# Optimization experiments

Measured on AMD Instinct MI355X. Metric: run time of the kernel, lower is better.

The kernel has to match this reference:

```python
import jax, jax.numpy as jnp
import numpy as np
from jax import lax

B, L = 128, 256
DW, DC = 100, 30
H = 400          # hidden_size (bidirectional total)
HD = H // 2      # per-direction hidden
NT = 18          # tag vocab size (BIOES)
VW, VC = 400000, 50000


def setup_inputs():
    key = jax.random.key(0)
    ks = iter(jax.random.split(key, 64))
    rn = lambda shape, s=0.1: jax.random.normal(next(ks), shape, jnp.float32) * s
    inp = {
        "words": jax.random.randint(next(ks), (B, L), 0, VW),
        "cap_words": jax.random.randint(next(ks), (B, L), 0, VC),
        "seq_len": jax.random.randint(next(ks), (B,), L // 2, L + 1),
        "target": jax.random.randint(next(ks), (B, L), 0, NT),
        "word_emb": rn((VW, DW)),
        "char_emb": rn((VC, DC)),
    }
    for l, din in ((0, DW + DC), (1, H)):
        for d in ("f", "b"):
            inp[f"W_ih_l{l}{d}"] = rn((4 * HD, din))
            inp[f"W_hh_l{l}{d}"] = rn((4 * HD, HD))
            inp[f"b_ih_l{l}{d}"] = rn((4 * HD,))
            inp[f"b_hh_l{l}{d}"] = rn((4 * HD,))
    inp["Wf"], inp["bf"] = rn((NT, HD)), jnp.zeros((NT,), jnp.float32)
    inp["Wb"], inp["bb"] = rn((NT, HD)), jnp.zeros((NT,), jnp.float32)
    inp["trans"] = rn((NT, NT))
    return inp


def _lstm_dir(x, W_ih, W_hh, b_ih, b_hh):
    # x: [B, L, D] -> hidden states [B, L, HD]; torch gate order i, f, g, o
    Bsz = x.shape[0]
    def step(carry, xt):
        h, c = carry
        g = xt @ W_ih.T + b_ih + h @ W_hh.T + b_hh
        i, f, gg, o = jnp.split(g, 4, axis=-1)
        c = jax.nn.sigmoid(f) * c + jax.nn.sigmoid(i) * jnp.tanh(gg)
        h = jax.nn.sigmoid(o) * jnp.tanh(c)
        return (h, c), h
    init = (jnp.zeros((Bsz, HD), x.dtype), jnp.zeros((Bsz, HD), x.dtype))
    _, hs = lax.scan(step, init, jnp.swapaxes(x, 0, 1))
    return jnp.swapaxes(hs, 0, 1)


def _rev(x, seq_len):
    # reverse each sequence within its true length (padding stays in place),
    # emulating pack_padded_sequence semantics for the backward direction
    t = jnp.arange(x.shape[1])[None, :]
    idx = jnp.where(t < seq_len[:, None], seq_len[:, None] - 1 - t, t)
    return jnp.take_along_axis(x, idx[:, :, None], axis=1)


def _crf_nll(logits, tags, mask, trans):
    # normalizer: forward algorithm, logsumexp scan over time with mask
    def step(alpha, inp):
        emit, m = inp  # emit: [B, NT], m: [B] bool
        new = jax.nn.logsumexp(alpha[:, :, None] + trans[None] + emit[:, None, :], axis=1)
        return jnp.where(m[:, None], new, alpha), None
    emits = jnp.swapaxes(logits, 0, 1)  # [L, B, NT]
    ms = jnp.swapaxes(mask, 0, 1)
    alpha, _ = lax.scan(step, emits[0], (emits[1:], ms[1:]))
    z = jax.nn.logsumexp(alpha, axis=1)
    # gold path score
    mf = mask.astype(logits.dtype)
    emit_sc = jnp.take_along_axis(logits, tags[:, :, None], axis=2)[:, :, 0]
    gold = jnp.sum(emit_sc * mf, axis=1) + jnp.sum(trans[tags[:, :-1], tags[:, 1:]] * mf[:, 1:], axis=1)
    return z - gold  # per-sample negative log-likelihood, shape [B]


def _model(words, cap_words, seq_len, target, word_emb, char_emb,
           W_ih_l0f, W_hh_l0f, b_ih_l0f, b_hh_l0f, W_ih_l0b, W_hh_l0b, b_ih_l0b, b_hh_l0b,
           W_ih_l1f, W_hh_l1f, b_ih_l1f, b_hh_l1f, W_ih_l1b, W_hh_l1b, b_ih_l1b, b_hh_l1b,
           Wf, bf, Wb, bb, trans):
    mask = jnp.arange(L)[None, :] < seq_len[:, None]  # [B, L] bool
    mf = mask.astype(jnp.float32)[:, :, None]
    x = jnp.concatenate([word_emb[words], char_emb[cap_words]], axis=-1)
    layers = (((W_ih_l0f, W_hh_l0f, b_ih_l0f, b_hh_l0f), (W_ih_l0b, W_hh_l0b, b_ih_l0b, b_hh_l0b)),
              ((W_ih_l1f, W_hh_l1f, b_ih_l1f, b_hh_l1f), (W_ih_l1b, W_hh_l1b, b_ih_l1b, b_hh_l1b)))
    h = x
    for fp, bp in layers:
        fwd = _lstm_dir(h, *fp)
        bwd = _rev(_lstm_dir(_rev(h, seq_len), *bp), seq_len)
        h = jnp.concatenate([fwd, bwd], axis=-1) * mf  # zero padded steps like packed LSTM
    forwards, backwards = h[..., :HD], h[..., HD:]
    logits = forwards @ Wf.T + bf + backwards @ Wb.T + bb
    return _crf_nll(logits, target, mask, trans)


def reference(words, cap_words, seq_len, target, word_emb, char_emb,
              W_ih_l0f, W_hh_l0f, b_ih_l0f, b_hh_l0f, W_ih_l0b, W_hh_l0b, b_ih_l0b, b_hh_l0b,
              W_ih_l1f, W_hh_l1f, b_ih_l1f, b_hh_l1f, W_ih_l1b, W_hh_l1b, b_ih_l1b, b_hh_l1b,
              Wf, bf, Wb, bb, trans):
    return _model(words, cap_words, seq_len, target, word_emb, char_emb,
                  W_ih_l0f, W_hh_l0f, b_ih_l0f, b_hh_l0f, W_ih_l0b, W_hh_l0b, b_ih_l0b, b_hh_l0b,
                  W_ih_l1f, W_hh_l1f, b_ih_l1f, b_hh_l1f, W_ih_l1b, W_hh_l1b, b_ih_l1b, b_hh_l1b,
                  Wf, bf, Wb, bb, trans)
```

## Files before the change

### kernel.cpp

```cpp
#include <hip/hip_runtime.h>
#include <math.h>

#define B_   128
#define L_   256
#define DW_  100
#define DC_  30
#define HD_  200
#define NT_  18
#define SG   4
#define KP0  160
#define KP1  416
#define WLP  424

typedef _Float16 half8 __attribute__((ext_vector_type(8)));
typedef _Float16 half4 __attribute__((ext_vector_type(4)));
typedef float    f32x4 __attribute__((ext_vector_type(4)));

__device__ __forceinline__ float frcp_(float x) { return __builtin_amdgcn_rcpf(x); }
__device__ __forceinline__ float sigm_(float x) { return frcp_(1.0f + __expf(-x)); }
__device__ __forceinline__ float tanh_(float x) { return 1.0f - 2.0f * frcp_(1.0f + __expf(2.0f * x)); }

__device__ __forceinline__ void barrier_lgkm() {
    asm volatile("s_waitcnt lgkmcnt(0)" ::: "memory");
    __builtin_amdgcn_s_barrier();
    asm volatile("" ::: "memory");
}

__global__ __launch_bounds__(128) void k_sortperm(const int* __restrict__ seq_len,
                                                  int* __restrict__ perm) {
    __shared__ int s[B_];
    int i = threadIdx.x;
    s[i] = seq_len[i];
    __syncthreads();
    int key = s[i], r = 0;
    for (int j = 0; j < B_; j++) {
        int v = s[j];
        r += (v < key) || (v == key && j < i);
    }
    perm[r] = i;
}

__global__ void k_embed(const int* __restrict__ words, const int* __restrict__ caps,
                        const float* __restrict__ wemb, const float* __restrict__ cemb,
                        _Float16* __restrict__ x) {
    int pos = blockIdx.x;
    int w = words[pos], c = caps[pos];
    _Float16* xp = x + (size_t)pos * KP0;
    for (int t = threadIdx.x; t < KP0; t += blockDim.x) {
        float v = 0.f;
        if (t < DW_) v = wemb[(size_t)w * DW_ + t];
        else if (t < DW_ + DC_) v = cemb[(size_t)c * DC_ + (t - DW_)];
        xp[t] = (_Float16)v;
    }
}

__global__ void k_perm_ih16(const float* __restrict__ src, _Float16* __restrict__ dst,
                            int K, int Kpad, int colOff) {
    int i = blockIdx.x * blockDim.x + threadIdx.x;
    if (i >= 800 * Kpad) return;
    int r = i / Kpad, k = i - r * Kpad;
    int jh = r % 200, g = r / 200;
    int col = colOff + (jh << 2) + g;
    dst[(size_t)col * Kpad + k] = (k < K) ? (_Float16)src[(size_t)r * K + k] : (_Float16)0.f;
}

__global__ void k_bias_perm(const float* bi_f, const float* bh_f,
                            const float* bi_b, const float* bh_b, float* bias) {
    int j = blockIdx.x * blockDim.x + threadIdx.x;
    if (j >= 1600) return;
    int dir = j / 800, r = j - dir * 800;
    int col = dir * 800 + ((r % 200) << 2) + (r / 200);
    bias[col] = dir ? (bi_b[r] + bh_b[r]) : (bi_f[r] + bh_f[r]);
}

__global__ void k_wlog(const float* __restrict__ Wf, const float* __restrict__ bfv,
                       const float* __restrict__ Wb, const float* __restrict__ bbv,
                       _Float16* __restrict__ wlB, float* __restrict__ blog) {
    int i = blockIdx.x * blockDim.x + threadIdx.x;
    if (i < 32 * WLP) {
        int n = i / WLP, k = i - n * WLP;
        float v = 0.f;
        if (n < NT_ && k < 400) v = (k < HD_) ? Wf[n * HD_ + k] : Wb[n * HD_ + (k - HD_)];
        wlB[i] = (_Float16)v;
    }
    if (i < NT_) blog[i] = bfv[i] + bbv[i];
}

__global__ __launch_bounds__(256) void k_gemm16(const _Float16* __restrict__ A,
                                                const _Float16* __restrict__ Bt,
                                                const float* __restrict__ bias,
                                                _Float16* __restrict__ C,
                                                int Kpad) {
    __shared__ __align__(16) _Float16 smem[128 * 72];
    _Float16* sA = smem;
    _Float16* sB = smem + 128 * 40;
    const int tid = threadIdx.x;
    const int w = tid >> 6, l = tid & 63, l15 = l & 15, lq = l >> 4;
    const int m0 = blockIdx.y * 128, n0 = blockIdx.x * 64;
    const int rw = (w >> 1) * 64, cw = (w & 1) * 32;
    f32x4 acc[4][2];
    #pragma unroll
    for (int i = 0; i < 4; i++)
        #pragma unroll
        for (int j = 0; j < 2; j++) acc[i][j] = f32x4{0.f, 0.f, 0.f, 0.f};

    for (int k0 = 0; k0 < Kpad; k0 += 32) {
        {
            int m = tid >> 1, c = (tid & 1) << 4;
            const _Float16* ap = A + (size_t)(m0 + m) * Kpad + k0 + c;
            *(half8*)&sA[m * 40 + c]     = *(const half8*)ap;
            *(half8*)&sA[m * 40 + c + 8] = *(const half8*)(ap + 8);
        }
        {
            int n = tid >> 2, k8 = (tid & 3) << 3;
            *(half8*)&sB[n * 40 + k8] = *(const half8*)&Bt[(size_t)(n0 + n) * Kpad + k0 + k8];
        }
        __syncthreads();
        half8 aF[4], bF[2];
        #pragma unroll
        for (int i = 0; i < 4; i++) aF[i] = *(const half8*)&sA[(rw + i * 16 + l15) * 40 + lq * 8];
        #pragma unroll
        for (int j = 0; j < 2; j++) bF[j] = *(const half8*)&sB[(cw + j * 16 + l15) * 40 + lq * 8];
        #pragma unroll
        for (int i = 0; i < 4; i++)
            #pragma unroll
            for (int j = 0; j < 2; j++)
                acc[i][j] = __builtin_amdgcn_mfma_f32_16x16x32_f16(aF[i], bF[j], acc[i][j], 0, 0, 0);
        __syncthreads();
    }

    #pragma unroll
    for (int j = 0; j < 2; j++) {
        int nl = cw + j * 16 + l15;
        float bv = bias[n0 + nl];
        #pragma unroll
        for (int i = 0; i < 4; i++) {
            int row = rw + i * 16 + lq * 4;
            #pragma unroll
            for (int r = 0; r < 4; r++)
                smem[(row + r) * 72 + nl] = (_Float16)(acc[i][j][r] + bv);
        }
    }
    __syncthreads();
    {
        int row = tid >> 1, hh = tid & 1;
        const _Float16* src = &smem[row * 72 + hh * 32];
        _Float16* dst = C + (size_t)(m0 + row) * 1600 + n0 + hh * 32;
        #pragma unroll
        for (int k = 0; k < 4; k++)
            *(half8*)(dst + k * 8) = *(const half8*)(src + k * 8);
    }
}

__global__ __launch_bounds__(512) void k_scan10(const _Float16* __restrict__ gates,
                                                const float* __restrict__ Whh_f,
                                                const float* __restrict__ Whh_b,
                                                const int* __restrict__ seq_len,
                                                const int* __restrict__ perm,
                                                _Float16* __restrict__ hout, int ldH) {
    const int dir = blockIdx.x & 1;
    const int b0  = (blockIdx.x >> 1) * SG;
    const int tid = threadIdx.x;
    const int w   = tid >> 6;
    const int l   = tid & 63;
    const int l15 = l & 15;
    const int lq  = l >> 4;

    __shared__ __align__(16) _Float16 hA[2][16 * 232];
    __shared__ __align__(16) _Float16 bEx[2 * 7 * 512];
    __shared__ __align__(16) float    gD[8 * 448];
    __shared__ int ssl[SG];
    __shared__ int spb[SG];

    const float* W = dir ? Whh_b : Whh_f;
    const int nT = (w < 2) ? 7 : 6;
    const int nCell = nT * 16;

    half8 Breg[6][7];
    #pragma unroll
    for (int i = 0; i < 6; i++) {
        int n  = (w * 6 + i) * 16 + l15;
        int jh = n >> 2, g = n & 3;
        const float* Wr = W + (size_t)(g * 200 + jh) * 200;
        #pragma unroll
        for (int kt = 0; kt < 7; kt++) {
            int k0 = kt * 32 + lq * 8;
            half8 f;
            #pragma unroll
            for (int j = 0; j < 8; j++) {
                int k = k0 + j;
                f[j] = (k < 200) ? (_Float16)Wr[k] : (_Float16)0.f;
            }
            Breg[i][kt] = f;
        }
    }
    if (w < 2) {
        int n  = (48 + w) * 16 + l15;
        int jh = n >> 2, g = n & 3;
        const float* Wr = W + (size_t)(g * 200 + jh) * 200;
        for (int kt = 0; kt < 7; kt++) {
            int k0 = kt * 32 + lq * 8;
            half8 f;
            for (int j = 0; j < 8; j++) {
                int k = k0 + j;
                f[j] = (k < 200) ? (_Float16)Wr[k] : (_Float16)0.f;
            }
            *(half8*)&bEx[(w * 7 + kt) * 512 + l * 8] = f;
        }
    }
    for (int i = tid; i < 2 * 16 * 232; i += 512) (&hA[0][0])[i] = (_Float16)0.f;
    if (tid < SG) {
        int ob = perm[b0 + tid];
        spb[tid] = ob;
        ssl[tid] = seq_len[ob];
    }

    const int  v    = tid;
    const bool stv  = v < 400;
    const int  m_st = v / 100;
    const int  u_st = v - m_st * 100;

    const int cA = l;
    const int iA = cA >> 4, qA = (cA >> 2) & 3, mA = cA & 3;
    const int tgA = (iA < 6) ? (w * 6 + iA) : (48 + w);
    const int hcA = tgA * 4 + qA;
    const int cB = l + 64;
    const int iB = cB >> 4, qB = (cB >> 2) & 3, mB = cB & 3;
    const bool vB = cB < nCell;
    const int tgB = (iB < 6) ? (w * 6 + iB) : (48 + w);
    const int hcB = tgB * 4 + qB;
    float csA = 0.f, csB = 0.f;

    __syncthreads();

    const int slmax = max(max(ssl[0], ssl[1]), max(ssl[2], ssl[3]));

    const int slA = ssl[mA];
    const int slB = ssl[mB];
    const int slb_st = stv ? ssl[m_st] : 0;
    const _Float16* gA_base = gates + ((size_t)spb[mA] * L_) * 1600 + dir * 800 + 4 * hcA;
    const _Float16* gB_base = gates + ((size_t)spb[mB] * L_) * 1600 + dir * 800 + 4 * hcB;
    _Float16* hout_base = stv ? (hout + (size_t)spb[m_st] * L_ * ldH + dir * HD_ + 2 * u_st)
                              : hout;

    auto rowOf = [&](int t, int sl) -> int {
        return dir ? ((t < sl) ? sl - 1 - t : t) : t;
    };

    half4 gA0, gA1, gB0, gB1;
    gA0 = *(const half4*)(gA_base + (size_t)rowOf(0, slA) * 1600);
    gA1 = *(const half4*)(gA_base + (size_t)rowOf(1, slA) * 1600);
    if (vB) {
        gB0 = *(const half4*)(gB_base + (size_t)rowOf(0, slB) * 1600);
        gB1 = *(const half4*)(gB_base + (size_t)rowOf(1, slB) * 1600);
    }

    const f32x4 Cz = {0.f, 0.f, 0.f, 0.f};
    for (int t = 0; t < slmax; t++) {
        const int p = t & 1;

        if (t > 0 && stv) {
            int tp = t - 1;
            int row = dir ? ((tp < slb_st) ? slb_st - 1 - tp : tp) : tp;
            unsigned int val = (tp < slb_st) ? *(const unsigned int*)&hA[p][m_st * 232 + 2 * u_st] : 0u;
            *(unsigned int*)(hout_base + (size_t)row * ldH) = val;
        }

        f32x4 C[7];
        #pragma unroll
        for (int i = 0; i < 7; i++) C[i] = Cz;
        #pragma unroll
        for (int kt = 0; kt < 7; kt++) {
            half8 hF = *(const half8*)&hA[p][l15 * 232 + kt * 32 + lq * 8];
            #pragma unroll
            for (int i = 0; i < 6; i++)
                C[i] = __builtin_amdgcn_mfma_f32_16x16x32_f16(Breg[i][kt], hF, C[i], 0, 0, 0);
            if (w < 2) {
                half8 bF = *(const half8*)&bEx[(w * 7 + kt) * 512 + l * 8];
                C[6] = __builtin_amdgcn_mfma_f32_16x16x32_f16(bF, hF, C[6], 0, 0, 0);
            }
        }

        if (l15 < 4) {
            #pragma unroll
            for (int i = 0; i < 6; i++)
                *(f32x4*)&gD[w * 448 + (i * 16 + lq * 4 + l15) * 4] = C[i];
            if (w < 2)
                *(f32x4*)&gD[w * 448 + (6 * 16 + lq * 4 + l15) * 4] = C[6];
        }

        {
            f32x4 gv = *(const f32x4*)&gD[w * 448 + cA * 4];
            float xi = gv[0] + (float)gA0[0];
            float xf = gv[1] + (float)gA0[1];
            float xg = gv[2] + (float)gA0[2];
            float xo = gv[3] + (float)gA0[3];
            float cn = sigm_(xf) * csA + sigm_(xi) * tanh_(xg);
            csA = cn;
            hA[1 - p][mA * 232 + hcA] = (_Float16)(sigm_(xo) * tanh_(cn));
        }
        if (vB) {
            f32x4 gv = *(const f32x4*)&gD[w * 448 + cB * 4];
            float xi = gv[0] + (float)gB0[0];
            float xf = gv[1] + (float)gB0[1];
            float xg = gv[2] + (float)gB0[2];
            float xo = gv[3] + (float)gB0[3];
            float cn = sigm_(xf) * csB + sigm_(xi) * tanh_(xg);
            csB = cn;
            hA[1 - p][mB * 232 + hcB] = (_Float16)(sigm_(xo) * tanh_(cn));
        }

        gA0 = gA1;
        gB0 = gB1;
        if (t + 2 < L_) {
            gA1 = *(const half4*)(gA_base + (size_t)rowOf(t + 2, slA) * 1600);
            if (vB) gB1 = *(const half4*)(gB_base + (size_t)rowOf(t + 2, slB) * 1600);
        }

        barrier_lgkm();
    }
    if (stv) {
        int tp = slmax - 1;
        int row = dir ? ((tp < slb_st) ? slb_st - 1 - tp : tp) : tp;
        unsigned int val = (tp < slb_st) ? *(const unsigned int*)&hA[slmax & 1][m_st * 232 + 2 * u_st] : 0u;
        *(unsigned int*)(hout_base + (size_t)row * ldH) = val;
    }
    if (stv) {
        for (int tp = slmax; tp < L_; tp++)
            *(unsigned int*)(hout_base + (size_t)tp * ldH) = 0u;
    }
}

__global__ __launch_bounds__(256) void k_logits(const _Float16* __restrict__ h1,
                                                const _Float16* __restrict__ wlB,
                                                const float* __restrict__ blog,
                                                float* __restrict__ logits) {
    __shared__ __align__(16) _Float16 sW[32 * WLP];
    const int tid = threadIdx.x;
    const int w = tid >> 6, l = tid & 63, l15 = l & 15, lq = l >> 4;
    for (int i = tid; i < 32 * WLP / 8; i += 256)
        ((half8*)sW)[i] = ((const half8*)wlB)[i];
    __syncthreads();

    const int m0 = blockIdx.x * 64 + w * 16;
    const half8 hz = {0, 0, 0, 0, 0, 0, 0, 0};
    f32x4 acc0 = {0.f, 0.f, 0.f, 0.f}, acc1 = {0.f, 0.f, 0.f, 0.f};
    const _Float16* arow = h1 + (size_t)(m0 + l15) * 400;
    #pragma unroll
    for (int kt = 0; kt < 13; kt++) {
        int col = kt * 32 + lq * 8;
        half8 aF = (col < 400) ? *(const half8*)(arow + col) : hz;
        half8 bF0 = *(const half8*)&sW[l15 * WLP + col];
        half8 bF1 = *(const half8*)&sW[(16 + l15) * WLP + col];
        acc0 = __builtin_amdgcn_mfma_f32_16x16x32_f16(aF, bF0, acc0, 0, 0, 0);
        acc1 = __builtin_amdgcn_mfma_f32_16x16x32_f16(aF, bF1, acc1, 0, 0, 0);
    }
    {
        int n = l15;
        float bv = blog[n];
        #pragma unroll
        for (int r = 0; r < 4; r++)
            logits[(size_t)(m0 + lq * 4 + r) * NT_ + n] = acc0[r] + bv;
    }
    if (16 + l15 < NT_) {
        int n = 16 + l15;
        float bv = blog[n];
        #pragma unroll
        for (int r = 0; r < 4; r++)
            logits[(size_t)(m0 + lq * 4 + r) * NT_ + n] = acc1[r] + bv;
    }
}

__global__ __launch_bounds__(64) void k_crf(const float* __restrict__ logits,
                                            const int* __restrict__ target,
                                            const int* __restrict__ seq_len,
                                            const float* __restrict__ trans,
                                            float* __restrict__ out) {
    int b = blockIdx.x, tid = threadIdx.x;
    __shared__ float alpha[NT_];
    int sl = seq_len[b];
    const float* lg = logits + (size_t)b * L_ * NT_;
    const int* tg = target + (size_t)b * L_;

    const bool act = tid < 54;
    const int c = tid / 18, j = tid - c * 18;

    float Tl[6];
    #pragma unroll
    for (int k = 0; k < 6; k++)
        Tl[k] = act ? trans[(6 * c + k) * NT_ + j] : 0.f;

    float gacc = 0.f;
    for (int t = tid; t < L_; t += 64) {
        if (t < sl) {
            gacc += lg[t * NT_ + tg[t]];
            if (t >= 1) gacc += trans[tg[t - 1] * NT_ + tg[t]];
        }
    }
    #pragma unroll
    for (int off = 32; off; off >>= 1) gacc += __shfl_down(gacc, off);
    float gold = __shfl(gacc, 0);

    if (tid < NT_) alpha[tid] = lg[tid];

    const int src1 = (c < 2) ? tid + 18 : tid - 36;
    const int src2 = (c == 0) ? tid + 36 : tid - 18;

    for (int t = 1; t < sl; t++) {
        float m = -1e30f, s = 0.f;
        if (act) {
            float v0 = alpha[6 * c + 0] + Tl[0];
            float v1 = alpha[6 * c + 1] + Tl[1];
            float v2 = alpha[6 * c + 2] + Tl[2];
            float v3 = alpha[6 * c + 3] + Tl[3];
            float v4 = alpha[6 * c + 4] + Tl[4];
            float v5 = alpha[6 * c + 5] + Tl[5];
            m = fmaxf(fmaxf(fmaxf(v0, v1), fmaxf(v2, v3)), fmaxf(v4, v5));
            s = __expf(v0 - m) + __expf(v1 - m) + __expf(v2 - m) +
                __expf(v3 - m) + __expf(v4 - m) + __expf(v5 - m);
        }
        float m1 = __shfl(m, src1), s1 = __shfl(s, src1);
        float m2 = __shfl(m, src2), s2 = __shfl(s, src2);
        if (act && c == 0) {
            float M = fmaxf(m, fmaxf(m1, m2));
            float S = s * __expf(m - M) + s1 * __expf(m1 - M) + s2 * __expf(m2 - M);
            alpha[j] = M + __logf(S) + lg[t * NT_ + j];
        }
    }
    if (tid == 0) {
        float mx = -1e30f;
        for (int i = 0; i < NT_; i++) mx = fmaxf(mx, alpha[i]);
        float s = 0.f;
        for (int i = 0; i < NT_; i++) s += __expf(alpha[i] - mx);
        out[b] = (mx + __logf(s)) - gold;
    }
}

extern "C" void kernel_launch(void* const* d_in, const int* in_sizes, int n_in,
                              void* d_out, int out_size, void* d_ws, size_t ws_size,
                              hipStream_t stream) {
    const int*   words  = (const int*)d_in[0];
    const int*   caps   = (const int*)d_in[1];
    const int*   seq    = (const int*)d_in[2];
    const int*   target = (const int*)d_in[3];
    const float* wemb   = (const float*)d_in[4];
    const float* cemb   = (const float*)d_in[5];
    const float* Wih0f  = (const float*)d_in[6];
    const float* Whh0f  = (const float*)d_in[7];
    const float* bih0f  = (const float*)d_in[8];
    const float* bhh0f  = (const float*)d_in[9];
    const float* Wih0b  = (const float*)d_in[10];
    const float* Whh0b  = (const float*)d_in[11];
    const float* bih0b  = (const float*)d_in[12];
    const float* bhh0b  = (const float*)d_in[13];
    const float* Wih1f  = (const float*)d_in[14];
    const float* Whh1f  = (const float*)d_in[15];
    const float* bih1f  = (const float*)d_in[16];
    const float* bhh1f  = (const float*)d_in[17];
    const float* Wih1b  = (const float*)d_in[18];
    const float* Whh1b  = (const float*)d_in[19];
    const float* bih1b  = (const float*)d_in[20];
    const float* bhh1b  = (const float*)d_in[21];
    const float* Wf     = (const float*)d_in[22];
    const float* bfv    = (const float*)d_in[23];
    const float* Wb     = (const float*)d_in[24];
    const float* bbv    = (const float*)d_in[25];
    const float* trans  = (const float*)d_in[26];

    char* base = (char*)d_ws;
    _Float16* gatesH = (_Float16*)(base + 0);
    _Float16* xbuf   = (_Float16*)(base + 104857600);
    _Float16* h0b    = (_Float16*)(base + 115343360);
    _Float16* h1b    = xbuf;
    float* logitsb   = (float*)(base + 142606336);
    _Float16* wihT0  = (_Float16*)(base + 144965632);
    _Float16* wihT1  = (_Float16*)(base + 145477632);
    float* bias0     = (float*)(base + 146808832);
    float* bias1     = (float*)(base + 146815232);
    _Float16* wlB    = (_Float16*)(base + 146821632);
    float* blog      = (float*)(base + 146850432);
    int*   permb     = (int*)(base + 146850560);

    k_perm_ih16<<<(800 * KP0 + 255) / 256, 256, 0, stream>>>(Wih0f, wihT0, 130, KP0, 0);
    k_perm_ih16<<<(800 * KP0 + 255) / 256, 256, 0, stream>>>(Wih0b, wihT0, 130, KP0, 800);
    k_perm_ih16<<<(800 * KP1 + 255) / 256, 256, 0, stream>>>(Wih1f, wihT1, 400, KP1, 0);
    k_perm_ih16<<<(800 * KP1 + 255) / 256, 256, 0, stream>>>(Wih1b, wihT1, 400, KP1, 800);
    k_bias_perm<<<7, 256, 0, stream>>>(bih0f, bhh0f, bih0b, bhh0b, bias0);
    k_bias_perm<<<7, 256, 0, stream>>>(bih1f, bhh1f, bih1b, bhh1b, bias1);
    k_wlog<<<(32 * WLP + 255) / 256, 256, 0, stream>>>(Wf, bfv, Wb, bbv, wlB, blog);
    k_sortperm<<<1, 128, 0, stream>>>(seq, permb);

    k_embed<<<B_ * L_, 128, 0, stream>>>(words, caps, wemb, cemb, xbuf);

    hipMemsetAsync(h0b, 0, (size_t)32768 * KP1 * sizeof(_Float16), stream);

    k_gemm16<<<dim3(25, 256), 256, 0, stream>>>(xbuf, wihT0, bias0, gatesH, KP0);
    k_scan10<<<(B_ / SG) * 2, 512, 0, stream>>>(gatesH, Whh0f, Whh0b, seq, permb, h0b, KP1);

    k_gemm16<<<dim3(25, 256), 256, 0, stream>>>(h0b, wihT1, bias1, gatesH, KP1);
    k_scan10<<<(B_ / SG) * 2, 512, 0, stream>>>(gatesH, Whh1f, Whh1b, seq, permb, h1b, 400);

    k_logits<<<(B_ * L_) / 64, 256, 0, stream>>>(h1b, wlB, blog, logitsb);
    k_crf<<<B_, 64, 0, stream>>>(logitsb, target, seq, trans, (float*)d_out);
}
```

Baseline: 1.368 ms.

## Split recurrent LSTM scan across 16 waves with three gate tiles each

The recurrent scan kernel now runs 1024 threads per block instead of 512. Each wave keeps 3 W_hh tiles in registers instead of 6, and each lane updates one cell instead of two. This halves the serial MFMA chain and the gate nonlinearity work each wave does per timestep, which shortens the latency-bound critical path of the recurrence. In exchange, the per-step block-wide barrier spans twice as many waves, and the lower register budget per thread at 1024 threads could cause spills.

```diff
diff --git a/kernel.cpp b/kernel.cpp
--- a/kernel.cpp
+++ b/kernel.cpp
@@ -152,12 +152,12 @@
     }
 }
 
-__global__ __launch_bounds__(512) void k_scan10(const _Float16* __restrict__ gates,
-                                                const float* __restrict__ Whh_f,
-                                                const float* __restrict__ Whh_b,
-                                                const int* __restrict__ seq_len,
-                                                const int* __restrict__ perm,
-                                                _Float16* __restrict__ hout, int ldH) {
+__global__ __launch_bounds__(1024) void k_scan14(const _Float16* __restrict__ gates,
+                                                 const float* __restrict__ Whh_f,
+                                                 const float* __restrict__ Whh_b,
+                                                 const int* __restrict__ seq_len,
+                                                 const int* __restrict__ perm,
+                                                 _Float16* __restrict__ hout, int ldH) {
     const int dir = blockIdx.x & 1;
     const int b0  = (blockIdx.x >> 1) * SG;
     const int tid = threadIdx.x;
@@ -168,18 +168,18 @@
 
     __shared__ __align__(16) _Float16 hA[2][16 * 232];
     __shared__ __align__(16) _Float16 bEx[2 * 7 * 512];
-    __shared__ __align__(16) float    gD[8 * 448];
+    __shared__ __align__(16) float    gD[16 * 256];
     __shared__ int ssl[SG];
     __shared__ int spb[SG];
 
     const float* W = dir ? Whh_b : Whh_f;
-    const int nT = (w < 2) ? 7 : 6;
+    const int nT = (w < 2) ? 4 : 3;
     const int nCell = nT * 16;
 
-    half8 Breg[6][7];
-    #pragma unroll
-    for (int i = 0; i < 6; i++) {
-        int n  = (w * 6 + i) * 16 + l15;
+    half8 Breg[3][7];
+    #pragma unroll
+    for (int i = 0; i < 3; i++) {
+        int n  = (w * 3 + i) * 16 + l15;
         int jh = n >> 2, g = n & 3;
         const float* Wr = W + (size_t)(g * 200 + jh) * 200;
         #pragma unroll
@@ -208,7 +208,7 @@
             *(half8*)&bEx[(w * 7 + kt) * 512 + l * 8] = f;
         }
     }
-    for (int i = tid; i < 2 * 16 * 232; i += 512) (&hA[0][0])[i] = (_Float16)0.f;
+    for (int i = tid; i < 2 * 16 * 232; i += 1024) (&hA[0][0])[i] = (_Float16)0.f;
     if (tid < SG) {
         int ob = perm[b0 + tid];
         spb[tid] = ob;
@@ -221,25 +221,19 @@
     const int  u_st = v - m_st * 100;
 
     const int cA = l;
+    const bool vA = cA < nCell;
     const int iA = cA >> 4, qA = (cA >> 2) & 3, mA = cA & 3;
-    const int tgA = (iA < 6) ? (w * 6 + iA) : (48 + w);
+    const int tgA = (iA < 3) ? (w * 3 + iA) : (48 + w);
     const int hcA = tgA * 4 + qA;
-    const int cB = l + 64;
-    const int iB = cB >> 4, qB = (cB >> 2) & 3, mB = cB & 3;
-    const bool vB = cB < nCell;
-    const int tgB = (iB < 6) ? (w * 6 + iB) : (48 + w);
-    const int hcB = tgB * 4 + qB;
-    float csA = 0.f, csB = 0.f;
+    float csA = 0.f;
 
     __syncthreads();
 
     const int slmax = max(max(ssl[0], ssl[1]), max(ssl[2], ssl[3]));
 
     const int slA = ssl[mA];
-    const int slB = ssl[mB];
     const int slb_st = stv ? ssl[m_st] : 0;
     const _Float16* gA_base = gates + ((size_t)spb[mA] * L_) * 1600 + dir * 800 + 4 * hcA;
-    const _Float16* gB_base = gates + ((size_t)spb[mB] * L_) * 1600 + dir * 800 + 4 * hcB;
     _Float16* hout_base = stv ? (hout + (size_t)spb[m_st] * L_ * ldH + dir * HD_ + 2 * u_st)
                               : hout;
 
@@ -247,12 +241,10 @@
         return dir ? ((t < sl) ? sl - 1 - t : t) : t;
     };
 
-    half4 gA0, gA1, gB0, gB1;
-    gA0 = *(const half4*)(gA_base + (size_t)rowOf(0, slA) * 1600);
-    gA1 = *(const half4*)(gA_base + (size_t)rowOf(1, slA) * 1600);
-    if (vB) {
-        gB0 = *(const half4*)(gB_base + (size_t)rowOf(0, slB) * 1600);
-        gB1 = *(const half4*)(gB_base + (size_t)rowOf(1, slB) * 1600);
+    half4 gA0, gA1;
+    if (vA) {
+        gA0 = *(const half4*)(gA_base + (size_t)rowOf(0, slA) * 1600);
+        gA1 = *(const half4*)(gA_base + (size_t)rowOf(1, slA) * 1600);
     }
 
     const f32x4 Cz = {0.f, 0.f, 0.f, 0.f};
@@ -266,31 +258,31 @@
             *(unsigned int*)(hout_base + (size_t)row * ldH) = val;
         }
 
-        f32x4 C[7];
-        #pragma unroll
-        for (int i = 0; i < 7; i++) C[i] = Cz;
+        f32x4 C[4];
+        #pragma unroll
+        for (int i = 0; i < 4; i++) C[i] = Cz;
         #pragma unroll
         for (int kt = 0; kt < 7; kt++) {
             half8 hF = *(const half8*)&hA[p][l15 * 232 + kt * 32 + lq * 8];
             #pragma unroll
-            for (int i = 0; i < 6; i++)
+            for (int i = 0; i < 3; i++)
                 C[i] = __builtin_amdgcn_mfma_f32_16x16x32_f16(Breg[i][kt], hF, C[i], 0, 0, 0);
             if (w < 2) {
                 half8 bF = *(const half8*)&bEx[(w * 7 + kt) * 512 + l * 8];
-                C[6] = __builtin_amdgcn_mfma_f32_16x16x32_f16(bF, hF, C[6], 0, 0, 0);
+                C[3] = __builtin_amdgcn_mfma_f32_16x16x32_f16(bF, hF, C[3], 0, 0, 0);
             }
         }
 
         if (l15 < 4) {
             #pragma unroll
-            for (int i = 0; i < 6; i++)
-                *(f32x4*)&gD[w * 448 + (i * 16 + lq * 4 + l15) * 4] = C[i];
+            for (int i = 0; i < 3; i++)
+                *(f32x4*)&gD[w * 256 + (i * 16 + lq * 4 + l15) * 4] = C[i];
             if (w < 2)
-                *(f32x4*)&gD[w * 448 + (6 * 16 + lq * 4 + l15) * 4] = C[6];
-        }
-
-        {
-            f32x4 gv = *(const f32x4*)&gD[w * 448 + cA * 4];
+                *(f32x4*)&gD[w * 256 + (3 * 16 + lq * 4 + l15) * 4] = C[3];
+        }
+
+        if (vA) {
+            f32x4 gv = *(const f32x4*)&gD[w * 256 + cA * 4];
             float xi = gv[0] + (float)gA0[0];
             float xf = gv[1] + (float)gA0[1];
             float xg = gv[2] + (float)gA0[2];
@@ -299,23 +291,10 @@
             csA = cn;
             hA[1 - p][mA * 232 + hcA] = (_Float16)(sigm_(xo) * tanh_(cn));
         }
-        if (vB) {
-            f32x4 gv = *(const f32x4*)&gD[w * 448 + cB * 4];
-            float xi = gv[0] + (float)gB0[0];
-            float xf = gv[1] + (float)gB0[1];
-            float xg = gv[2] + (float)gB0[2];
-            float xo = gv[3] + (float)gB0[3];
-            float cn = sigm_(xf) * csB + sigm_(xi) * tanh_(xg);
-            csB = cn;
-            hA[1 - p][mB * 232 + hcB] = (_Float16)(sigm_(xo) * tanh_(cn));
-        }
 
         gA0 = gA1;
-        gB0 = gB1;
-        if (t + 2 < L_) {
+        if (vA && t + 2 < L_)
             gA1 = *(const half4*)(gA_base + (size_t)rowOf(t + 2, slA) * 1600);
-            if (vB) gB1 = *(const half4*)(gB_base + (size_t)rowOf(t + 2, slB) * 1600);
-        }
 
         barrier_lgkm();
     }
@@ -495,10 +474,10 @@
     hipMemsetAsync(h0b, 0, (size_t)32768 * KP1 * sizeof(_Float16), stream);
 
     k_gemm16<<<dim3(25, 256), 256, 0, stream>>>(xbuf, wihT0, bias0, gatesH, KP0);
-    k_scan10<<<(B_ / SG) * 2, 512, 0, stream>>>(gatesH, Whh0f, Whh0b, seq, permb, h0b, KP1);
+    k_scan14<<<(B_ / SG) * 2, 1024, 0, stream>>>(gatesH, Whh0f, Whh0b, seq, permb, h0b, KP1);
 
     k_gemm16<<<dim3(25, 256), 256, 0, stream>>>(h0b, wihT1, bias1, gatesH, KP1);
-    k_scan10<<<(B_ / SG) * 2, 512, 0, stream>>>(gatesH, Whh1f, Whh1b, seq, permb, h1b, 400);
+    k_scan14<<<(B_ / SG) * 2, 1024, 0, stream>>>(gatesH, Whh1f, Whh1b, seq, permb, h1b, 400);
 
     k_logits<<<(B_ * L_) / 64, 256, 0, stream>>>(h1b, wlB, blog, logitsb);
     k_crf<<<B_, 64, 0, stream>>>(logitsb, target, seq, trans, (float*)d_out);
```

After: 1.394 ms. No clear change (+1.9%).
